# Optimization experiments

Measured on AMD Instinct MI355X. Metric: run time of the kernel, lower is better.

## Reference

```python
import jax, jax.numpy as jnp
import numpy as np

N = 40000
E = 640000
D = 256
H = 8
DH = D // H
DFF = 4 * D
SCALE = D ** (-0.5)
EPS = 1e-5


def layernorm(x, g, b):
    mu = jnp.mean(x, axis=-1, keepdims=True)
    var = jnp.mean(jnp.square(x - mu), axis=-1, keepdims=True)
    return (x - mu) * jax.lax.rsqrt(var + EPS) * g + b


def setup_inputs() -> dict:
    key = jax.random.key(0)
    ks = jax.random.split(key, 12)
    inv = 1.0 / np.sqrt(D)
    invf = 1.0 / np.sqrt(DFF)
    return {
        "triplet_h": jax.random.normal(ks[0], (N, D), dtype=jnp.float32),
        "src": jax.random.randint(ks[1], (E,), 0, N, dtype=jnp.int32),
        "dst": jax.random.randint(ks[2], (E,), 0, N, dtype=jnp.int32),
        "Wqkv": jax.random.uniform(ks[3], (D, 3 * D), jnp.float32, -inv, inv),
        "bqkv": jax.random.uniform(ks[4], (3 * D,), jnp.float32, -inv, inv),
        "ln_attn_g": jnp.ones((D,), jnp.float32),
        "ln_attn_b": jnp.zeros((D,), jnp.float32),
        "ln_res_g": jnp.ones((D,), jnp.float32),
        "ln_res_b": jnp.zeros((D,), jnp.float32),
        "W_in": jax.random.uniform(ks[5], (D, DFF), jnp.float32, -inv, inv),
        "b_in": jax.random.uniform(ks[6], (DFF,), jnp.float32, -inv, inv),
        "W_out": jax.random.uniform(ks[7], (DFF, D), jnp.float32, -invf, invf),
        "b_out": jax.random.uniform(ks[8], (D,), jnp.float32, -invf, invf),
    }


def reference(triplet_h, src, dst, Wqkv, bqkv, ln_attn_g, ln_attn_b,
              ln_res_g, ln_res_b, W_in, b_in, W_out, b_out):
    n = triplet_h.shape[0]
    h = layernorm(triplet_h, ln_attn_g, ln_attn_b)
    qkv = (h @ Wqkv + bqkv).reshape(n, 3, H, DH)
    q = qkv[:, 0] * SCALE          # [N, H, DH]
    k = qkv[:, 1]
    v = qkv[:, 2]

    # per-edge attention logits: dot(Q_src, K_dst) per head -> [E, H]
    scores = jnp.einsum('ehd,ehd->eh', q[src], k[dst])
    # segment softmax over incoming edges of each dst node
    m = jax.ops.segment_max(scores, dst, num_segments=n)      # [N, H]
    e = jnp.exp(scores - m[dst])
    s = jax.ops.segment_sum(e, dst, num_segments=n)           # [N, H]
    sa = e / s[dst]                                           # [E, H]

    # weighted scatter-sum of src V into dst nodes
    he = (v[src] * sa[:, :, None]).reshape(-1, D)             # [E, D]
    agg = jax.ops.segment_sum(he, dst, num_segments=n)        # [N, D]

    # Residual block: x = triplet_h + agg; x + MLP(LN(x))
    x = triplet_h + agg
    y = layernorm(x, ln_res_g, ln_res_b)
    y = jax.nn.gelu(y @ W_in + b_in, approximate=False) @ W_out + b_out
    return x + y
```

## Files before the change

kernel.cpp:

```cpp
#include <hip/hip_runtime.h>
#include <math.h>

#define N_NODES 40000
#define M_PAD   40064
#define N_EDGES 640000
#define D       256
#define H       8
#define DFF     1024
#define D3      768
#define ATT_SCALE 0.0625f
#define LN_EPS  1e-5f

typedef __attribute__((ext_vector_type(8))) short short8;
typedef __attribute__((ext_vector_type(4))) float f32x4;
typedef __attribute__((ext_vector_type(2))) float f32x2;

__device__ __forceinline__ unsigned short f2bf(float f) {
    unsigned int u = __builtin_bit_cast(unsigned int, f);
    u = (u + 0x7FFF + ((u >> 16) & 1)) >> 16;
    return (unsigned short)u;
}
__device__ __forceinline__ float bf2f(unsigned short u) {
    return __builtin_bit_cast(float, (unsigned int)u << 16);
}

__device__ __forceinline__ float fast_gelu(float x) {
    const float z  = fabsf(x) * 0.70710678118654752f;
    const float t  = __builtin_amdgcn_rcpf(1.0f + 0.3275911f * z);
    float p = 1.061405429f;
    p = p * t - 1.453152027f;
    p = p * t + 1.421413741f;
    p = p * t - 0.284496736f;
    p = p * t + 0.254829592f;
    const float e  = __expf(-z * z);
    const float ea = 1.0f - p * t * e;
    const float er = (x < 0.0f) ? -ea : ea;
    return 0.5f * x * (1.0f + er);
}

#define GLOAD_LDS16(g, l) \
    __builtin_amdgcn_global_load_lds((const __attribute__((address_space(1))) void*)(g), \
                                     (__attribute__((address_space(3))) void*)(l), 16, 0, 0)

#if __has_builtin(__builtin_amdgcn_cvt_pk_fp8_f32) && __has_builtin(__builtin_amdgcn_cvt_pk_f32_fp8)
#define HW_FP8 1
#else
#define HW_FP8 0
__device__ __forceinline__ unsigned char enc_e4m3(float f) {
    unsigned int u = __builtin_bit_cast(unsigned int, f);
    unsigned int s = (u >> 24) & 0x80;
    float a = fabsf(f);
    if (a >= 0x1p-6f) {
        unsigned int bits = __builtin_bit_cast(unsigned int, a);
        unsigned int q = bits >> 20;
        unsigned int rem = bits & 0xFFFFFu;
        q += (rem > 0x80000u) || ((rem == 0x80000u) && (q & 1));
        q -= 960;
        if (q > 126) q = 126;
        return (unsigned char)(s | q);
    }
    float t = a * 512.0f;
    unsigned int r = (unsigned int)rintf(t);
    return (unsigned char)(s | r);
}
__device__ __forceinline__ float dec_e4m3(unsigned int v) {
    unsigned int em = v & 0x7f;
    float n = __builtin_bit_cast(float, (em << 20) + 0x3C000000u);
    float r = (em >= 8) ? n : (float)em * 0x1p-9f;
    return (v & 0x80) ? -r : r;
}
#endif

__device__ __forceinline__ unsigned int pack4_e4m3(float a, float b, float c, float d) {
#if HW_FP8
    unsigned int w = (unsigned int)__builtin_amdgcn_cvt_pk_fp8_f32(a, b, 0, false);
    w = (unsigned int)__builtin_amdgcn_cvt_pk_fp8_f32(c, d, (int)w, true);
    return w;
#else
    return (unsigned int)enc_e4m3(a) | ((unsigned int)enc_e4m3(b) << 8)
         | ((unsigned int)enc_e4m3(c) << 16) | ((unsigned int)enc_e4m3(d) << 24);
#endif
}
__device__ __forceinline__ void dec4_e4m3(unsigned int w, float& a, float& b, float& c, float& d) {
#if HW_FP8
    f32x2 lo = __builtin_amdgcn_cvt_pk_f32_fp8((int)w, false);
    f32x2 hi = __builtin_amdgcn_cvt_pk_f32_fp8((int)w, true);
    a = lo[0]; b = lo[1]; c = hi[0]; d = hi[1];
#else
    a = dec_e4m3(w & 0xff); b = dec_e4m3((w >> 8) & 0xff);
    c = dec_e4m3((w >> 16) & 0xff); d = dec_e4m3(w >> 24);
#endif
}

__global__ __launch_bounds__(256) void ln_bf_kernel(const float* __restrict__ in,
                                                    const float* __restrict__ g,
                                                    const float* __restrict__ b,
                                                    unsigned short* __restrict__ out)
{
    const int row  = blockIdx.x * 4 + (threadIdx.x >> 6);
    const int lane = threadIdx.x & 63;
    const size_t off = (((size_t)(row >> 4) * (D / 8) + (lane >> 1)) * 16 + (row & 15)) * 8
                       + (lane & 1) * 4;
    if (row >= N_NODES) {
        ushort4 z = {0, 0, 0, 0};
        *reinterpret_cast<ushort4*>(out + off) = z;
        return;
    }
    const float4 v = *reinterpret_cast<const float4*>(in + (size_t)row * D + lane * 4);
    float s  = v.x + v.y + v.z + v.w;
    float s2 = v.x * v.x + v.y * v.y + v.z * v.z + v.w * v.w;
#pragma unroll
    for (int o = 32; o > 0; o >>= 1) {
        s  += __shfl_xor(s,  o, 64);
        s2 += __shfl_xor(s2, o, 64);
    }
    const float mu  = s * (1.0f / D);
    const float var = s2 * (1.0f / D) - mu * mu;
    const float rs  = rsqrtf(var + LN_EPS);
    const float4 gg = *reinterpret_cast<const float4*>(g + lane * 4);
    const float4 bb = *reinterpret_cast<const float4*>(b + lane * 4);
    ushort4 o4;
    o4.x = f2bf((v.x - mu) * rs * gg.x + bb.x);
    o4.y = f2bf((v.y - mu) * rs * gg.y + bb.y);
    o4.z = f2bf((v.z - mu) * rs * gg.z + bb.z);
    o4.w = f2bf((v.w - mu) * rs * gg.w + bb.w);
    *reinterpret_cast<ushort4*>(out + off) = o4;
}

template <int K, int N>
__device__ __forceinline__ void pack_body(const float* __restrict__ W,
                                          unsigned short* __restrict__ Wpk, int blk)
{
    const int idx = blk * 256 + threadIdx.x;
    const int ni  = idx & 15;
    const int kc  = (idx >> 4) % (K / 8);
    const int nt  = idx / (16 * (K / 8));
    const int n   = nt * 16 + ni;
    unsigned short o[8];
#pragma unroll
    for (int i = 0; i < 8; ++i)
        o[i] = f2bf(W[(size_t)(kc * 8 + i) * N + n]);
    *reinterpret_cast<short8*>(Wpk + (size_t)idx * 8) = *reinterpret_cast<short8*>(o);
}

__global__ __launch_bounds__(256) void pack_all_kernel(const float* __restrict__ Wqkv,
                                                       const float* __restrict__ W_in,
                                                       const float* __restrict__ W_out,
                                                       unsigned short* __restrict__ pq,
                                                       unsigned short* __restrict__ pi,
                                                       unsigned short* __restrict__ po)
{
    const int b = blockIdx.x;
    if (b < 96)       pack_body<D, D3 >(Wqkv, pq, b);
    else if (b < 224) pack_body<D, DFF>(W_in, pi, b - 96);
    else              pack_body<DFF, D>(W_out, po, b - 224);
}

template <int EPI, int K, int N>
__global__ __launch_bounds__(256, 4) void mfma_gemm_kernel(const unsigned short* __restrict__ A,
                                                           const unsigned short* __restrict__ Bpk,
                                                           const float* __restrict__ bias,
                                                           void* __restrict__ Cout,
                                                           void* __restrict__ Cout2,
                                                           void* __restrict__ Cout3,
                                                           const float* __restrict__ Xadd)
{
    constexpr int C = N / 128;
    constexpr int P = M_PAD / 128;

    const int bid = blockIdx.x;
    const int xcd = bid & 7;
    const int t   = bid >> 3;
    const int c   = t % C;
    const int p   = (t / C) * 8 + xcd;
    if (p >= P) return;

    __shared__ unsigned short As[4096];
    __shared__ unsigned short Bs[4096];

    const int tid  = threadIdx.x;
    const int wave = tid >> 6;
    const int lane = tid & 63;
    const int row0 = p * 128;
    const int col0 = c * 128;
    const int wm   = (wave >> 1) * 64;
    const int wn   = (wave & 1) * 64;
    const int g    = lane >> 4;
    const int q    = lane & 15;

    f32x4 acc[4][4] = {};

    const int fragoff = g * 128 + q * 8;

    for (int k0 = 0; k0 < K; k0 += 32) {
        const int kq = k0 >> 3;
#pragma unroll
        for (int cc = 0; cc < 2; ++cc) {
            const int mt = wave * 2 + cc;
            const unsigned short* gA =
                A + ((size_t)(row0 / 16 + mt) * (K / 8) + kq) * 128 + lane * 8;
            GLOAD_LDS16(gA, &As[mt * 512]);
            const unsigned short* gB =
                Bpk + ((size_t)(col0 / 16 + mt) * (K / 8) + kq) * 128 + lane * 8;
            GLOAD_LDS16(gB, &Bs[mt * 512]);
        }
        __syncthreads();

        short8 af[4], bf[4];
#pragma unroll
        for (int i = 0; i < 4; ++i) {
            af[i] = *reinterpret_cast<const short8*>(&As[(wm / 16 + i) * 512 + fragoff]);
            bf[i] = *reinterpret_cast<const short8*>(&Bs[(wn / 16 + i) * 512 + fragoff]);
        }
#pragma unroll
        for (int i = 0; i < 4; ++i)
#pragma unroll
            for (int j = 0; j < 4; ++j)
                acc[i][j] = __builtin_amdgcn_mfma_f32_16x16x32_bf16(bf[j], af[i], acc[i][j], 0, 0, 0);
        __syncthreads();
    }

    if constexpr (EPI == 0) {
        if (col0 < 256) {
            unsigned char* q8 = (unsigned char*)Cout;
#pragma unroll
            for (int j = 0; j < 4; ++j) {
                const int nb = col0 + wn + j * 16 + g * 4;
                const float4 bz = *reinterpret_cast<const float4*>(bias + nb);
#pragma unroll
                for (int i = 0; i < 4; ++i) {
                    const int r = row0 + wm + i * 16 + q;
                    if (r >= N_NODES) continue;
                    const unsigned int w = pack4_e4m3(acc[i][j][0] + bz.x, acc[i][j][1] + bz.y,
                                                      acc[i][j][2] + bz.z, acc[i][j][3] + bz.w);
                    *reinterpret_cast<unsigned int*>(q8 + (size_t)r * 256 + nb) = w;
                }
            }
        } else if (col0 < 512) {
            unsigned short* kb = (unsigned short*)Cout2;
#pragma unroll
            for (int j = 0; j < 4; ++j) {
                const int nb = col0 + wn + j * 16 + g * 4;
                const float4 bz = *reinterpret_cast<const float4*>(bias + nb);
#pragma unroll
                for (int i = 0; i < 4; ++i) {
                    const int r = row0 + wm + i * 16 + q;
                    if (r >= N_NODES) continue;
                    ushort4 u;
                    u.x = f2bf(acc[i][j][0] + bz.x);
                    u.y = f2bf(acc[i][j][1] + bz.y);
                    u.z = f2bf(acc[i][j][2] + bz.z);
                    u.w = f2bf(acc[i][j][3] + bz.w);
                    *reinterpret_cast<ushort4*>(kb + (size_t)r * 256 + (nb - 256)) = u;
                }
            }
        } else {
            unsigned char* v8 = (unsigned char*)Cout3;
#pragma unroll
            for (int j = 0; j < 4; ++j) {
                const int nb = col0 + wn + j * 16 + g * 4;
                const float4 bz = *reinterpret_cast<const float4*>(bias + nb);
#pragma unroll
                for (int i = 0; i < 4; ++i) {
                    const int r = row0 + wm + i * 16 + q;
                    if (r >= N_NODES) continue;
                    const unsigned int w = pack4_e4m3(acc[i][j][0] + bz.x, acc[i][j][1] + bz.y,
                                                      acc[i][j][2] + bz.z, acc[i][j][3] + bz.w);
                    *reinterpret_cast<unsigned int*>(v8 + (size_t)r * 256 + (nb - 512)) = w;
                }
            }
        }
    } else if constexpr (EPI == 1) {
#pragma unroll
        for (int j = 0; j < 4; ++j) {
            const int nb = col0 + wn + j * 16 + g * 4;
            const float4 bz = *reinterpret_cast<const float4*>(bias + nb);
#pragma unroll
            for (int i = 0; i < 4; ++i) {
                const int r = row0 + wm + i * 16 + q;
                const float o0 = fast_gelu(acc[i][j][0] + bz.x);
                const float o1 = fast_gelu(acc[i][j][1] + bz.y);
                const float o2 = fast_gelu(acc[i][j][2] + bz.z);
                const float o3 = fast_gelu(acc[i][j][3] + bz.w);
                const size_t off = (((size_t)(r >> 4) * (N / 8) + (nb >> 3)) * 16
                                    + (r & 15)) * 8 + (nb & 7);
                ushort4 u;
                u.x = f2bf(o0); u.y = f2bf(o1); u.z = f2bf(o2); u.w = f2bf(o3);
                *reinterpret_cast<ushort4*>((unsigned short*)Cout + off) = u;
            }
        }
    } else {
#pragma unroll
        for (int j = 0; j < 4; ++j) {
            const int nb = col0 + wn + j * 16 + g * 4;
            const float4 bz = *reinterpret_cast<const float4*>(bias + nb);
#pragma unroll
            for (int i = 0; i < 4; ++i) {
                const int r = row0 + wm + i * 16 + q;
                if (r >= N_NODES) continue;
                const f32x4 xd = __builtin_nontemporal_load(
                    reinterpret_cast<const f32x4*>(Xadd + (size_t)r * N + nb));
                f32x4 ov;
                ov[0] = acc[i][j][0] + bz.x + xd[0];
                ov[1] = acc[i][j][1] + bz.y + xd[1];
                ov[2] = acc[i][j][2] + bz.z + xd[2];
                ov[3] = acc[i][j][3] + bz.w + xd[3];
                __builtin_nontemporal_store(ov,
                    reinterpret_cast<f32x4*>((float*)Cout + (size_t)r * N + nb));
            }
        }
    }
}

__global__ __launch_bounds__(256) void hist_kernel(const int* __restrict__ dst,
                                                   int* __restrict__ counts)
{
    const int i = blockIdx.x * 256 + threadIdx.x;
    atomicAdd(&counts[dst[i]], 1);
}

__global__ __launch_bounds__(1024) void scan_kernel(const int* __restrict__ counts,
                                                    int* __restrict__ rowptr,
                                                    int* __restrict__ cursor)
{
    const int PER = 40;
    const int tid  = threadIdx.x;
    const int base = tid * PER;
    const bool act = (base < N_NODES);
    int s = 0;
    if (act) {
#pragma unroll
        for (int i = 0; i < PER / 4; ++i) {
            const int4 c4 = *reinterpret_cast<const int4*>(counts + base + i * 4);
            s += (c4.x + c4.y) + (c4.z + c4.w);
        }
    }
    __shared__ int sm[1024];
    sm[tid] = s;
    __syncthreads();
    for (int off = 1; off < 1024; off <<= 1) {
        int t = (tid >= off) ? sm[tid - off] : 0;
        __syncthreads();
        sm[tid] += t;
        __syncthreads();
    }
    int run = sm[tid] - s;
    if (act) {
#pragma unroll
        for (int i = 0; i < PER / 4; ++i) {
            const int4 c4 = *reinterpret_cast<const int4*>(counts + base + i * 4);
            int4 r4;
            r4.x = run;
            r4.y = r4.x + c4.x;
            r4.z = r4.y + c4.y;
            r4.w = r4.z + c4.z;
            run  = r4.w + c4.w;
            *reinterpret_cast<int4*>(rowptr + base + i * 4) = r4;
            *reinterpret_cast<int4*>(cursor + base + i * 4) = r4;
        }
    }
    if (tid == 1023) rowptr[N_NODES] = sm[1023];
}

__global__ __launch_bounds__(256) void fill_kernel(const int* __restrict__ src,
                                                   const int* __restrict__ dst,
                                                   int* __restrict__ cursor,
                                                   int* __restrict__ srcs)
{
    const int e = blockIdx.x * 256 + threadIdx.x;
    const int pos = atomicAdd(&cursor[dst[e]], 1);
    if (pos >= 0 && pos < N_EDGES) srcs[pos] = src[e];
}

__global__ __launch_bounds__(256) void fused_attn_kernel(const unsigned char* __restrict__ qf8,
                                                         const unsigned short* __restrict__ kbf,
                                                         const unsigned char* __restrict__ vf8,
                                                         const int* __restrict__ srcs,
                                                         const int* __restrict__ rowptr,
                                                         const float* __restrict__ triplet_h,
                                                         const float* __restrict__ g,
                                                         const float* __restrict__ b,
                                                         float* __restrict__ x,
                                                         unsigned short* __restrict__ xn)
{
    const int node = blockIdx.x * 4 + (threadIdx.x >> 6);
    const int lane = threadIdx.x & 63;
    int beg = rowptr[node];
    int end = rowptr[node + 1];
    beg = max(0, min(beg, N_EDGES));
    end = max(beg, min(end, N_EDGES));
    const int deg = end - beg;

    const ushort4 ku = *reinterpret_cast<const ushort4*>(
        kbf + (size_t)node * 256 + lane * 4);
    const float k0 = bf2f(ku.x) * ATT_SCALE, k1 = bf2f(ku.y) * ATT_SCALE;
    const float k2 = bf2f(ku.z) * ATT_SCALE, k3 = bf2f(ku.w) * ATT_SCALE;

    float dsum = 0.0f;
    float4 acc = {0.0f, 0.0f, 0.0f, 0.0f};

    for (int base = 0; base < deg; base += 64) {
        const int cnt = min(64, deg - base);
        const int idx = base + lane;
        const int sv = (idx < deg) ? srcs[beg + idx] : 0;
        int j = 0;
        for (; j + 4 <= cnt; j += 4) {
            const int s0 = __builtin_amdgcn_readlane(sv, j);
            const int s1 = __builtin_amdgcn_readlane(sv, j + 1);
            const int s2 = __builtin_amdgcn_readlane(sv, j + 2);
            const int s3 = __builtin_amdgcn_readlane(sv, j + 3);
            const unsigned int qa = *reinterpret_cast<const unsigned int*>(qf8 + (size_t)s0 * 256 + lane * 4);
            const unsigned int qb = *reinterpret_cast<const unsigned int*>(qf8 + (size_t)s1 * 256 + lane * 4);
            const unsigned int qc = *reinterpret_cast<const unsigned int*>(qf8 + (size_t)s2 * 256 + lane * 4);
            const unsigned int qd = *reinterpret_cast<const unsigned int*>(qf8 + (size_t)s3 * 256 + lane * 4);
            const unsigned int va = *reinterpret_cast<const unsigned int*>(vf8 + (size_t)s0 * 256 + lane * 4);
            const unsigned int vb = *reinterpret_cast<const unsigned int*>(vf8 + (size_t)s1 * 256 + lane * 4);
            const unsigned int vc = *reinterpret_cast<const unsigned int*>(vf8 + (size_t)s2 * 256 + lane * 4);
            const unsigned int vd = *reinterpret_cast<const unsigned int*>(vf8 + (size_t)s3 * 256 + lane * 4);
            float a0, a1, a2, a3;
            dec4_e4m3(qa, a0, a1, a2, a3);
            float p0 = a0 * k0 + a1 * k1 + a2 * k2 + a3 * k3;
            dec4_e4m3(qb, a0, a1, a2, a3);
            float p1 = a0 * k0 + a1 * k1 + a2 * k2 + a3 * k3;
            dec4_e4m3(qc, a0, a1, a2, a3);
            float p2 = a0 * k0 + a1 * k1 + a2 * k2 + a3 * k3;
            dec4_e4m3(qd, a0, a1, a2, a3);
            float p3 = a0 * k0 + a1 * k1 + a2 * k2 + a3 * k3;
            p0 += __shfl_xor(p0, 1, 64); p1 += __shfl_xor(p1, 1, 64);
            p2 += __shfl_xor(p2, 1, 64); p3 += __shfl_xor(p3, 1, 64);
            p0 += __shfl_xor(p0, 2, 64); p1 += __shfl_xor(p1, 2, 64);
            p2 += __shfl_xor(p2, 2, 64); p3 += __shfl_xor(p3, 2, 64);
            p0 += __shfl_xor(p0, 4, 64); p1 += __shfl_xor(p1, 4, 64);
            p2 += __shfl_xor(p2, 4, 64); p3 += __shfl_xor(p3, 4, 64);
            const float w0 = __expf(p0), w1 = __expf(p1), w2 = __expf(p2), w3 = __expf(p3);
            float v0, v1, v2, v3;
            dec4_e4m3(va, v0, v1, v2, v3);
            acc.x += w0 * v0; acc.y += w0 * v1; acc.z += w0 * v2; acc.w += w0 * v3;
            dec4_e4m3(vb, v0, v1, v2, v3);
            acc.x += w1 * v0; acc.y += w1 * v1; acc.z += w1 * v2; acc.w += w1 * v3;
            dec4_e4m3(vc, v0, v1, v2, v3);
            acc.x += w2 * v0; acc.y += w2 * v1; acc.z += w2 * v2; acc.w += w2 * v3;
            dec4_e4m3(vd, v0, v1, v2, v3);
            acc.x += w3 * v0; acc.y += w3 * v1; acc.z += w3 * v2; acc.w += w3 * v3;
            dsum += (w0 + w1) + (w2 + w3);
        }
        for (; j < cnt; ++j) {
            const int s0 = __builtin_amdgcn_readlane(sv, j);
            const unsigned int qa = *reinterpret_cast<const unsigned int*>(qf8 + (size_t)s0 * 256 + lane * 4);
            const unsigned int va = *reinterpret_cast<const unsigned int*>(vf8 + (size_t)s0 * 256 + lane * 4);
            float a0, a1, a2, a3;
            dec4_e4m3(qa, a0, a1, a2, a3);
            float p0 = a0 * k0 + a1 * k1 + a2 * k2 + a3 * k3;
            p0 += __shfl_xor(p0, 1, 64);
            p0 += __shfl_xor(p0, 2, 64);
            p0 += __shfl_xor(p0, 4, 64);
            const float w0 = __expf(p0);
            float v0, v1, v2, v3;
            dec4_e4m3(va, v0, v1, v2, v3);
            acc.x += w0 * v0; acc.y += w0 * v1; acc.z += w0 * v2; acc.w += w0 * v3;
            dsum += w0;
        }
    }
    const float inv = (deg > 0) ? 1.0f / dsum : 0.0f;

    const float4 th = *reinterpret_cast<const float4*>(
        triplet_h + (size_t)node * D + lane * 4);
    float4 xv;
    xv.x = th.x + acc.x * inv;
    xv.y = th.y + acc.y * inv;
    xv.z = th.z + acc.z * inv;
    xv.w = th.w + acc.w * inv;
    *reinterpret_cast<float4*>(x + (size_t)node * D + lane * 4) = xv;

    float s  = xv.x + xv.y + xv.z + xv.w;
    float s2 = xv.x * xv.x + xv.y * xv.y + xv.z * xv.z + xv.w * xv.w;
#pragma unroll
    for (int o = 32; o > 0; o >>= 1) {
        s  += __shfl_xor(s,  o, 64);
        s2 += __shfl_xor(s2, o, 64);
    }
    const float mu  = s * (1.0f / D);
    const float var = s2 * (1.0f / D) - mu * mu;
    const float rs  = rsqrtf(var + LN_EPS);
    const float4 gg = *reinterpret_cast<const float4*>(g + lane * 4);
    const float4 bb = *reinterpret_cast<const float4*>(b + lane * 4);
    ushort4 o4;
    o4.x = f2bf((xv.x - mu) * rs * gg.x + bb.x);
    o4.y = f2bf((xv.y - mu) * rs * gg.y + bb.y);
    o4.z = f2bf((xv.z - mu) * rs * gg.z + bb.z);
    o4.w = f2bf((xv.w - mu) * rs * gg.w + bb.w);
    const size_t off = (((size_t)(node >> 4) * (D / 8) + (lane >> 1)) * 16 + (node & 15)) * 8
                       + (lane & 1) * 4;
    *reinterpret_cast<ushort4*>(xn + off) = o4;
}

extern "C" void kernel_launch(void* const* d_in, const int* in_sizes, int n_in,
                              void* d_out, int out_size, void* d_ws, size_t ws_size,
                              hipStream_t stream)
{
    const float* triplet_h = (const float*)d_in[0];
    const int*   src       = (const int*)d_in[1];
    const int*   dst       = (const int*)d_in[2];
    const float* Wqkv      = (const float*)d_in[3];
    const float* bqkv      = (const float*)d_in[4];
    const float* ln_attn_g = (const float*)d_in[5];
    const float* ln_attn_b = (const float*)d_in[6];
    const float* ln_res_g  = (const float*)d_in[7];
    const float* ln_res_b  = (const float*)d_in[8];
    const float* W_in      = (const float*)d_in[9];
    const float* b_in      = (const float*)d_in[10];
    const float* W_out     = (const float*)d_in[11];
    const float* b_out     = (const float*)d_in[12];
    float* out = (float*)d_out;

    char* w = (char*)d_ws;
    unsigned short* bufA = (unsigned short*)w;
    w += (size_t)M_PAD * DFF * sizeof(unsigned short);
    unsigned short* h_xn = (unsigned short*)w;  w += (size_t)M_PAD * D * sizeof(unsigned short);
    float*          x    = (float*)w;           w += (size_t)N_NODES * D * sizeof(float);
    unsigned char*  qf8  = (unsigned char*)w;   w += (size_t)N_NODES * 256;
    unsigned char*  vf8  = (unsigned char*)w;   w += (size_t)N_NODES * 256;
    unsigned short* Wqkv_pk = (unsigned short*)w; w += (size_t)D * D3 * sizeof(unsigned short);
    unsigned short* Win_pk  = (unsigned short*)w; w += (size_t)D * DFF * sizeof(unsigned short);
    unsigned short* Wout_pk = (unsigned short*)w; w += (size_t)DFF * D * sizeof(unsigned short);
    int* counts = (int*)w;  w += (size_t)N_NODES * sizeof(int);
    int* rowptr = (int*)w;  w += (size_t)(N_NODES + 1) * sizeof(int);
    int* cursor = (int*)w;  w += (size_t)N_NODES * sizeof(int);
    int* srcs   = (int*)w;  w += (size_t)N_EDGES * sizeof(int);

    unsigned short* kbf = bufA;
    unsigned short* a1  = bufA;

    (void)hipMemsetAsync(counts, 0, (size_t)N_NODES * sizeof(int), stream);
    hist_kernel<<<N_EDGES / 256, 256, 0, stream>>>(dst, counts);
    scan_kernel<<<1, 1024, 0, stream>>>(counts, rowptr, cursor);
    fill_kernel<<<N_EDGES / 256, 256, 0, stream>>>(src, dst, cursor, srcs);

    pack_all_kernel<<<352, 256, 0, stream>>>(Wqkv, W_in, W_out, Wqkv_pk, Win_pk, Wout_pk);

    ln_bf_kernel<<<M_PAD / 4, 256, 0, stream>>>(triplet_h, ln_attn_g, ln_attn_b, h_xn);
    mfma_gemm_kernel<0, D, D3><<<((M_PAD / 128 + 7) / 8) * 8 * (D3 / 128), 256, 0, stream>>>(
        h_xn, Wqkv_pk, bqkv, qf8, kbf, vf8, nullptr);
    fused_attn_kernel<<<N_NODES / 4, 256, 0, stream>>>(qf8, kbf, vf8, srcs, rowptr, triplet_h,
                                                       ln_res_g, ln_res_b, x, h_xn);
    mfma_gemm_kernel<1, D, DFF><<<((M_PAD / 128 + 7) / 8) * 8 * (DFF / 128), 256, 0, stream>>>(
        h_xn, Win_pk, b_in, a1, nullptr, nullptr, nullptr);
    mfma_gemm_kernel<2, DFF, D><<<((M_PAD / 128 + 7) / 8) * 8 * (D / 128), 256, 0, stream>>>(
        a1, Wout_pk, b_out, out, nullptr, nullptr, x);

    (void)in_sizes; (void)n_in; (void)out_size; (void)ws_size;
}
```

Before: 385.2 us.

## Fuse FFN up-projection, GELU and down-projection into one kernel

Replaces the two separate MLP GEMM launches with a single fused kernel. Each block handles 64 rows and loops over 128-wide DFF chunks: it computes the up-projection with GELU into LDS, then immediately accumulates the down-projection. This avoids writing and re-reading the 40000x1024 bf16 intermediate through global memory. In exchange it reads operands straight from global memory without LDS staging for A and the weights, uses a smaller tile, and the 256-wide output accumulators raise register pressure, which may hurt MFMA efficiency.

```diff
diff --git a/kernel.cpp b/kernel.cpp
--- a/kernel.cpp
+++ b/kernel.cpp
@@ -162,8 +162,7 @@
                                                            const float* __restrict__ bias,
                                                            void* __restrict__ Cout,
                                                            void* __restrict__ Cout2,
-                                                           void* __restrict__ Cout3,
-                                                           const float* __restrict__ Xadd)
+                                                           void* __restrict__ Cout3)
 {
     constexpr int C = N / 128;
     constexpr int P = M_PAD / 128;
@@ -220,57 +219,8 @@
         __syncthreads();
     }
 
-    if constexpr (EPI == 0) {
-        if (col0 < 256) {
-            unsigned char* q8 = (unsigned char*)Cout;
-#pragma unroll
-            for (int j = 0; j < 4; ++j) {
-                const int nb = col0 + wn + j * 16 + g * 4;
-                const float4 bz = *reinterpret_cast<const float4*>(bias + nb);
-#pragma unroll
-                for (int i = 0; i < 4; ++i) {
-                    const int r = row0 + wm + i * 16 + q;
-                    if (r >= N_NODES) continue;
-                    const unsigned int w = pack4_e4m3(acc[i][j][0] + bz.x, acc[i][j][1] + bz.y,
-                                                      acc[i][j][2] + bz.z, acc[i][j][3] + bz.w);
-                    *reinterpret_cast<unsigned int*>(q8 + (size_t)r * 256 + nb) = w;
-                }
-            }
-        } else if (col0 < 512) {
-            unsigned short* kb = (unsigned short*)Cout2;
-#pragma unroll
-            for (int j = 0; j < 4; ++j) {
-                const int nb = col0 + wn + j * 16 + g * 4;
-                const float4 bz = *reinterpret_cast<const float4*>(bias + nb);
-#pragma unroll
-                for (int i = 0; i < 4; ++i) {
-                    const int r = row0 + wm + i * 16 + q;
-                    if (r >= N_NODES) continue;
-                    ushort4 u;
-                    u.x = f2bf(acc[i][j][0] + bz.x);
-                    u.y = f2bf(acc[i][j][1] + bz.y);
-                    u.z = f2bf(acc[i][j][2] + bz.z);
-                    u.w = f2bf(acc[i][j][3] + bz.w);
-                    *reinterpret_cast<ushort4*>(kb + (size_t)r * 256 + (nb - 256)) = u;
-                }
-            }
-        } else {
-            unsigned char* v8 = (unsigned char*)Cout3;
-#pragma unroll
-            for (int j = 0; j < 4; ++j) {
-                const int nb = col0 + wn + j * 16 + g * 4;
-                const float4 bz = *reinterpret_cast<const float4*>(bias + nb);
-#pragma unroll
-                for (int i = 0; i < 4; ++i) {
-                    const int r = row0 + wm + i * 16 + q;
-                    if (r >= N_NODES) continue;
-                    const unsigned int w = pack4_e4m3(acc[i][j][0] + bz.x, acc[i][j][1] + bz.y,
-                                                      acc[i][j][2] + bz.z, acc[i][j][3] + bz.w);
-                    *reinterpret_cast<unsigned int*>(v8 + (size_t)r * 256 + (nb - 512)) = w;
-                }
-            }
-        }
-    } else if constexpr (EPI == 1) {
+    if (col0 < 256) {
+        unsigned char* q8 = (unsigned char*)Cout;
 #pragma unroll
         for (int j = 0; j < 4; ++j) {
             const int nb = col0 + wn + j * 16 + g * 4;
@@ -278,18 +228,14 @@
 #pragma unroll
             for (int i = 0; i < 4; ++i) {
                 const int r = row0 + wm + i * 16 + q;
-                const float o0 = fast_gelu(acc[i][j][0] + bz.x);
-                const float o1 = fast_gelu(acc[i][j][1] + bz.y);
-                const float o2 = fast_gelu(acc[i][j][2] + bz.z);
-                const float o3 = fast_gelu(acc[i][j][3] + bz.w);
-                const size_t off = (((size_t)(r >> 4) * (N / 8) + (nb >> 3)) * 16
-                                    + (r & 15)) * 8 + (nb & 7);
-                ushort4 u;
-                u.x = f2bf(o0); u.y = f2bf(o1); u.z = f2bf(o2); u.w = f2bf(o3);
-                *reinterpret_cast<ushort4*>((unsigned short*)Cout + off) = u;
+                if (r >= N_NODES) continue;
+                const unsigned int w = pack4_e4m3(acc[i][j][0] + bz.x, acc[i][j][1] + bz.y,
+                                                  acc[i][j][2] + bz.z, acc[i][j][3] + bz.w);
+                *reinterpret_cast<unsigned int*>(q8 + (size_t)r * 256 + nb) = w;
             }
         }
-    } else {
+    } else if (col0 < 512) {
+        unsigned short* kb = (unsigned short*)Cout2;
 #pragma unroll
         for (int j = 0; j < 4; ++j) {
             const int nb = col0 + wn + j * 16 + g * 4;
@@ -298,16 +244,138 @@
             for (int i = 0; i < 4; ++i) {
                 const int r = row0 + wm + i * 16 + q;
                 if (r >= N_NODES) continue;
-                const f32x4 xd = __builtin_nontemporal_load(
-                    reinterpret_cast<const f32x4*>(Xadd + (size_t)r * N + nb));
-                f32x4 ov;
-                ov[0] = acc[i][j][0] + bz.x + xd[0];
-                ov[1] = acc[i][j][1] + bz.y + xd[1];
-                ov[2] = acc[i][j][2] + bz.z + xd[2];
-                ov[3] = acc[i][j][3] + bz.w + xd[3];
-                __builtin_nontemporal_store(ov,
-                    reinterpret_cast<f32x4*>((float*)Cout + (size_t)r * N + nb));
+                ushort4 u;
+                u.x = f2bf(acc[i][j][0] + bz.x);
+                u.y = f2bf(acc[i][j][1] + bz.y);
+                u.z = f2bf(acc[i][j][2] + bz.z);
+                u.w = f2bf(acc[i][j][3] + bz.w);
+                *reinterpret_cast<ushort4*>(kb + (size_t)r * 256 + (nb - 256)) = u;
             }
+        }
+    } else {
+        unsigned char* v8 = (unsigned char*)Cout3;
+#pragma unroll
+        for (int j = 0; j < 4; ++j) {
+            const int nb = col0 + wn + j * 16 + g * 4;
+            const float4 bz = *reinterpret_cast<const float4*>(bias + nb);
+#pragma unroll
+            for (int i = 0; i < 4; ++i) {
+                const int r = row0 + wm + i * 16 + q;
+                if (r >= N_NODES) continue;
+                const unsigned int w = pack4_e4m3(acc[i][j][0] + bz.x, acc[i][j][1] + bz.y,
+                                                  acc[i][j][2] + bz.z, acc[i][j][3] + bz.w);
+                *reinterpret_cast<unsigned int*>(v8 + (size_t)r * 256 + (nb - 512)) = w;
+            }
+        }
+    }
+}
+
+__global__ __launch_bounds__(256, 3) void fused_ffn_kernel(const unsigned short* __restrict__ A,
+                                                           const unsigned short* __restrict__ Wi,
+                                                           const unsigned short* __restrict__ Wo,
+                                                           const float* __restrict__ b_in,
+                                                           const float* __restrict__ b_out,
+                                                           const float* __restrict__ x,
+                                                           float* __restrict__ out)
+{
+    __shared__ unsigned short a1c[8192];
+
+    const int p    = blockIdx.x;
+    const int tid  = threadIdx.x;
+    const int wave = tid >> 6;
+    const int lane = tid & 63;
+    const int g    = lane >> 4;
+    const int q    = lane & 15;
+    const int wrow = (wave & 1) * 2;
+    const int wc1  = (wave >> 1) * 4;
+    const int wc2  = (wave >> 1) * 8;
+
+    f32x4 acc2[2][8] = {};
+
+#pragma unroll 1
+    for (int ch = 0; ch < 8; ++ch) {
+        f32x4 acc1[2][4] = {};
+#pragma unroll
+        for (int ks = 0; ks < 8; ++ks) {
+            const int kc = ks * 4 + g;
+            short8 ah[2], bw[4];
+#pragma unroll
+            for (int i = 0; i < 2; ++i)
+                ah[i] = *reinterpret_cast<const short8*>(
+                    A + ((size_t)(p * 4 + wrow + i) * 32 + kc) * 128 + q * 8);
+#pragma unroll
+            for (int j = 0; j < 4; ++j) {
+                const int nt = ch * 8 + wc1 + j;
+                bw[j] = *reinterpret_cast<const short8*>(
+                    Wi + ((size_t)nt * 32 + kc) * 128 + q * 8);
+            }
+#pragma unroll
+            for (int i = 0; i < 2; ++i)
+#pragma unroll
+                for (int j = 0; j < 4; ++j)
+                    acc1[i][j] = __builtin_amdgcn_mfma_f32_16x16x32_bf16(bw[j], ah[i], acc1[i][j], 0, 0, 0);
+        }
+        __syncthreads();
+
+#pragma unroll
+        for (int j = 0; j < 4; ++j) {
+            const int cb = (wc1 + j) * 16 + g * 4;
+            const float4 bz = *reinterpret_cast<const float4*>(b_in + ch * 128 + cb);
+            const int kc = cb >> 3;
+            const int ki = (g & 1) * 4;
+#pragma unroll
+            for (int i = 0; i < 2; ++i) {
+                ushort4 u;
+                u.x = f2bf(fast_gelu(acc1[i][j][0] + bz.x));
+                u.y = f2bf(fast_gelu(acc1[i][j][1] + bz.y));
+                u.z = f2bf(fast_gelu(acc1[i][j][2] + bz.z));
+                u.w = f2bf(fast_gelu(acc1[i][j][3] + bz.w));
+                *reinterpret_cast<ushort4*>(
+                    &a1c[(((wrow + i) * 16 + kc) * 16 + q) * 8 + ki]) = u;
+            }
+        }
+        __syncthreads();
+
+#pragma unroll
+        for (int ks = 0; ks < 4; ++ks) {
+            const int kc = ks * 4 + g;
+            short8 aa[2], bw[8];
+#pragma unroll
+            for (int i = 0; i < 2; ++i)
+                aa[i] = *reinterpret_cast<const short8*>(
+                    &a1c[(((wrow + i) * 16 + kc) * 16 + q) * 8]);
+#pragma unroll
+            for (int j = 0; j < 8; ++j) {
+                const int nt = wc2 + j;
+                const int kcg = ch * 16 + kc;
+                bw[j] = *reinterpret_cast<const short8*>(
+                    Wo + ((size_t)nt * 128 + kcg) * 128 + q * 8);
+            }
+#pragma unroll
+            for (int i = 0; i < 2; ++i)
+#pragma unroll
+                for (int j = 0; j < 8; ++j)
+                    acc2[i][j] = __builtin_amdgcn_mfma_f32_16x16x32_bf16(bw[j], aa[i], acc2[i][j], 0, 0, 0);
+        }
+    }
+
+#pragma unroll
+    for (int j = 0; j < 8; ++j) {
+        const int col = (wc2 + j) * 16 + g * 4;
+        const float4 bz = *reinterpret_cast<const float4*>(b_out + col);
+#pragma unroll
+        for (int i = 0; i < 2; ++i) {
+            const int r = p * 64 + (wrow + i) * 16 + q;
+            if (r >= N_NODES) continue;
+            const f32x4 xd = __builtin_nontemporal_load(
+                reinterpret_cast<const f32x4*>(x + (size_t)r * D + col));
+            f32x4 ov;
+            ov[0] = acc2[i][j][0] + bz.x + xd[0];
+            ov[1] = acc2[i][j][1] + bz.y + xd[1];
+            ov[2] = acc2[i][j][2] + bz.z + xd[2];
+            ov[3] = acc2[i][j][3] + bz.w + xd[3];
+            __builtin_nontemporal_store(ov,
+                reinterpret_cast<f32x4*>(out + (size_t)r * D + col));
         }
     }
 }
@@ -514,9 +582,8 @@
     float* out = (float*)d_out;
 
     char* w = (char*)d_ws;
-    unsigned short* bufA = (unsigned short*)w;
-    w += (size_t)M_PAD * DFF * sizeof(unsigned short);
     unsigned short* h_xn = (unsigned short*)w;  w += (size_t)M_PAD * D * sizeof(unsigned short);
+    unsigned short* kbf  = (unsigned short*)w;  w += (size_t)N_NODES * D * sizeof(unsigned short);
     float*          x    = (float*)w;           w += (size_t)N_NODES * D * sizeof(float);
     unsigned char*  qf8  = (unsigned char*)w;   w += (size_t)N_NODES * 256;
     unsigned char*  vf8  = (unsigned char*)w;   w += (size_t)N_NODES * 256;
@@ -528,9 +595,6 @@
     int* cursor = (int*)w;  w += (size_t)N_NODES * sizeof(int);
     int* srcs   = (int*)w;  w += (size_t)N_EDGES * sizeof(int);
 
-    unsigned short* kbf = bufA;
-    unsigned short* a1  = bufA;
-
     (void)hipMemsetAsync(counts, 0, (size_t)N_NODES * sizeof(int), stream);
     hist_kernel<<<N_EDGES / 256, 256, 0, stream>>>(dst, counts);
     scan_kernel<<<1, 1024, 0, stream>>>(counts, rowptr, cursor);
@@ -540,13 +604,10 @@
 
     ln_bf_kernel<<<M_PAD / 4, 256, 0, stream>>>(triplet_h, ln_attn_g, ln_attn_b, h_xn);
     mfma_gemm_kernel<0, D, D3><<<((M_PAD / 128 + 7) / 8) * 8 * (D3 / 128), 256, 0, stream>>>(
-        h_xn, Wqkv_pk, bqkv, qf8, kbf, vf8, nullptr);
+        h_xn, Wqkv_pk, bqkv, qf8, kbf, vf8);
     fused_attn_kernel<<<N_NODES / 4, 256, 0, stream>>>(qf8, kbf, vf8, srcs, rowptr, triplet_h,
                                                        ln_res_g, ln_res_b, x, h_xn);
-    mfma_gemm_kernel<1, D, DFF><<<((M_PAD / 128 + 7) / 8) * 8 * (DFF / 128), 256, 0, stream>>>(
-        h_xn, Win_pk, b_in, a1, nullptr, nullptr, nullptr);
-    mfma_gemm_kernel<2, DFF, D><<<((M_PAD / 128 + 7) / 8) * 8 * (D / 128), 256, 0, stream>>>(
-        a1, Wout_pk, b_out, out, nullptr, nullptr, x);
+    fused_ffn_kernel<<<M_PAD / 64, 256, 0, stream>>>(h_xn, Win_pk, Wout_pk, b_in, b_out, x, out);
 
     (void)in_sizes; (void)n_in; (void)out_size; (void)ws_size;
 }
```

Result: slower. 707.8 us (+83.7%).
